# Kernel optimization log

Measured on AMD Instinct MI355X. Metric: run time of the kernel, lower is better.

Reference implementation:

```python
import jax, jax.numpy as jnp
import numpy as np

B, N, F = 8, 8192, 64          # batch of graphs, nodes per graph, feature dim
E = 1_048_576                   # total edges (avg in-degree 16 over 65536 nodes)


def setup_inputs() -> dict:
    key = jax.random.key(0)
    k1, k2, k3 = jax.random.split(key, 3)
    input_features = jax.random.normal(k1, (B, N, F), dtype=jnp.float32)
    src = jax.random.randint(k2, (E,), 0, B * N, dtype=jnp.int64)
    dst = jax.random.randint(k3, (E,), 0, B * N, dtype=jnp.int64)
    return {"input_features": input_features, "src": src, "dst": dst}


def reference(input_features, src, dst):
    # copy_src message + mean mailbox reduction (DGL update_all semantics):
    # each node's new h = mean of h over its in-neighbors; zero-in-degree
    # nodes keep their old h.
    b, n, f = input_features.shape
    num_nodes = b * n
    h = input_features.reshape(num_nodes, f)          # flatten batched graph nodes
    msg = h[src]                                       # [E, F] gathered messages
    msum = jax.ops.segment_sum(msg, dst, num_segments=num_nodes)       # [num_nodes, F]
    deg = jax.ops.segment_sum(jnp.ones((src.shape[0],), h.dtype), dst,
                              num_segments=num_nodes)                  # [num_nodes]
    mean = msum / jnp.maximum(deg, 1.0)[:, None]
    h_new = jnp.where(deg[:, None] > 0, mean, h)
    return h_new.reshape(b, n, f)
```

## Files before the change

kernel.cpp:

```cpp
#include <hip/hip_runtime.h>


#define NBUCK 2048
#define NPBLK 256
#define NPT   8
#define GBLK  1024
#define PAIRCAP 2048
#define EPBMAX 4096

template <bool BF16>
__global__ __launch_bounds__(256) void k_build(
        const float* __restrict__ h,
        const int* __restrict__ src,
        const int* __restrict__ dst,
        unsigned int* __restrict__ pairs,
        unsigned short* __restrict__ offs,
        uint4* __restrict__ hbf,
        int E, int epb, int n8) {
    int t = threadIdx.x;
    int bid = blockIdx.x;

    if (bid >= NPBLK) {
        if (!BF16) return;
        int i = (bid - NPBLK) * 256 + t;
        if (i >= n8) return;
        const float4* h4 = (const float4*)h;
        float4 a = h4[2 * i], bq = h4[2 * i + 1];
        auto pk = [](float lo, float hi) {
            unsigned int ul = __float_as_uint(lo), uh = __float_as_uint(hi);
            unsigned int rl = (ul + 0x7FFFu + ((ul >> 16) & 1u)) >> 16;
            unsigned int rh = (uh + 0x7FFFu + ((uh >> 16) & 1u)) & 0xFFFF0000u;
            return rl | rh;
        };
        hbf[i] = make_uint4(pk(a.x, a.y), pk(a.z, a.w), pk(bq.x, bq.y), pk(bq.z, bq.w));
        return;
    }

    __shared__ unsigned int hist[NBUCK];
    __shared__ uint4 dstbuf4[EPBMAX / 4];
    __shared__ unsigned int wpart[4];
    for (int i = t; i < NBUCK; i += 256) hist[i] = 0u;
    __syncthreads();

    int base = bid * epb;
    int cnt = E - base; if (cnt > epb) cnt = epb; if (cnt < 0) cnt = 0;
    int nv = cnt >> 2;

    const int4* d4 = (const int4*)(dst + base);
    for (int i = t; i < nv; i += 256) {
        int4 d = d4[i];
        dstbuf4[i] = make_uint4((unsigned)d.x, (unsigned)d.y,
                                (unsigned)d.z, (unsigned)d.w);
        atomicAdd(&hist[((unsigned)d.x) >> 5], 1u);
        atomicAdd(&hist[((unsigned)d.y) >> 5], 1u);
        atomicAdd(&hist[((unsigned)d.z) >> 5], 1u);
        atomicAdd(&hist[((unsigned)d.w) >> 5], 1u);
    }
    for (int i = nv * 4 + t; i < cnt; i += 256)
        atomicAdd(&hist[((unsigned)dst[base + i]) >> 5], 1u);
    __syncthreads();

    unsigned int loc[NPT], lsum = 0u;
    #pragma unroll
    for (int i = 0; i < NPT; ++i) { loc[i] = hist[t * NPT + i]; lsum += loc[i]; }
    int lane = t & 63, wid = t >> 6;
    unsigned int x = lsum;
    #pragma unroll
    for (int off = 1; off < 64; off <<= 1) {
        unsigned int y = __shfl_up(x, off);
        if (lane >= off) x += y;
    }
    if (lane == 63) wpart[wid] = x;
    __syncthreads();
    if (wid == 0) {
        unsigned int w = (lane < 4) ? wpart[lane] : 0u;
        #pragma unroll
        for (int off = 1; off < 4; off <<= 1) {
            unsigned int y = __shfl_up(w, off);
            if (lane >= off) w += y;
        }
        if (lane < 4) wpart[lane] = w;
    }
    __syncthreads();
    unsigned int run = (wid ? wpart[wid - 1] : 0u) + x - lsum;

    size_t orow = (size_t)bid * (NBUCK + 1);
    #pragma unroll
    for (int i = 0; i < NPT; ++i) {
        offs[orow + t * NPT + i] = (unsigned short)run;
        hist[t * NPT + i] = (unsigned)base + run;
        run += loc[i];
    }
    if (t == 255) offs[orow + NBUCK] = (unsigned short)cnt;
    __syncthreads();

    const int4* s4 = (const int4*)(src + base);
    for (int i = t; i < nv; i += 256) {
        int4 s = s4[i];
        uint4 d = dstbuf4[i];
        unsigned int p0 = atomicAdd(&hist[d.x >> 5], 1u);
        pairs[p0] = (unsigned)s.x | ((d.x & 63u) << 16);
        unsigned int p1 = atomicAdd(&hist[d.y >> 5], 1u);
        pairs[p1] = (unsigned)s.y | ((d.y & 63u) << 16);
        unsigned int p2 = atomicAdd(&hist[d.z >> 5], 1u);
        pairs[p2] = (unsigned)s.z | ((d.z & 63u) << 16);
        unsigned int p3 = atomicAdd(&hist[d.w >> 5], 1u);
        pairs[p3] = (unsigned)s.w | ((d.w & 63u) << 16);
    }
    for (int i = nv * 4 + t; i < cnt; i += 256) {
        unsigned int d = (unsigned)dst[base + i];
        unsigned int s = (unsigned)src[base + i];
        unsigned int pos = atomicAdd(&hist[d >> 5], 1u);
        pairs[pos] = s | ((d & 63u) << 16);
    }
}

template <bool BF16>
__global__ __launch_bounds__(512) void k_gather(
        const float* __restrict__ h,
        const uint2* __restrict__ hbf,
        const unsigned int* __restrict__ pairs,
        const unsigned short* __restrict__ offs,
        float* __restrict__ out, int epb) {
    __shared__ unsigned int pairbuf[PAIRCAP];
    __shared__ unsigned short ssrc[PAIRCAP];
    __shared__ unsigned int hist[64], offl[64], cur[64];
    __shared__ unsigned int wpart[8];
    int t = threadIdx.x;
    int B = blockIdx.x;
    int g = (B & 7) * (GBLK / 8) + (B >> 3);
    int b2 = 2 * g;
    if (t < 64) hist[t] = 0u;

    unsigned int s0 = 0u, mycnt = 0u;
    if (t < NPBLK) {
        size_t orow = (size_t)t * (NBUCK + 1);
        s0 = offs[orow + b2];
        unsigned int s2 = offs[orow + b2 + 2];
        mycnt = s2 - s0;
    }

    int lane = t & 63, wid = t >> 6;
    unsigned int x = mycnt;
    #pragma unroll
    for (int off = 1; off < 64; off <<= 1) {
        unsigned int y = __shfl_up(x, off);
        if (lane >= off) x += y;
    }
    if (lane == 63) wpart[wid] = x;
    __syncthreads();
    if (wid == 0) {
        unsigned int w = (lane < 8) ? wpart[lane] : 0u;
        #pragma unroll
        for (int off = 1; off < 8; off <<= 1) {
            unsigned int y = __shfl_up(w, off);
            if (lane >= off) w += y;
        }
        if (lane < 8) wpart[lane] = w;
    }
    __syncthreads();
    unsigned int mypos = (wid ? wpart[wid - 1] : 0u) + x - mycnt;
    unsigned int cnt = min(wpart[7], (unsigned)PAIRCAP);
    if (mypos >= cnt) mycnt = 0u;
    else if (mypos + mycnt > cnt) mycnt = cnt - mypos;

    for (unsigned int k = 0; k < mycnt; ++k) {
        unsigned int pr = pairs[(size_t)t * epb + s0 + k];
        pairbuf[mypos + k] = pr;
        atomicAdd(&hist[pr >> 16], 1u);
    }
    __syncthreads();

    if (t < 64) {
        unsigned int v = hist[t];
        unsigned int xx = v;
        #pragma unroll
        for (int off = 1; off < 64; off <<= 1) {
            unsigned int y = __shfl_up(xx, off);
            if (t >= off) xx += y;
        }
        offl[t] = xx - v; cur[t] = xx - v;
    }
    __syncthreads();

    for (unsigned int i = t; i < cnt; i += 512u) {
        unsigned int p = pairbuf[i];
        unsigned int pos = atomicAdd(&cur[p >> 16], 1u);
        ssrc[pos] = (unsigned short)(p & 0xFFFFu);
    }
    __syncthreads();

    int w = t >> 6;
    int egrp = lane >> 4, fq = lane & 15;
    const float4* h4 = (const float4*)h;
    float4* out4 = (float4*)out;

    for (int np = 0; np < 4; ++np) {
        int na = w * 8 + np * 2;
        int nb = na + 1;
        unsigned int sa = offl[na], da = hist[na];
        unsigned int sb = offl[nb], db = hist[nb];
        float4 accA = make_float4(0.f, 0.f, 0.f, 0.f);
        float4 accB = make_float4(0.f, 0.f, 0.f, 0.f);
        unsigned int dmax = max(da, db);
        for (unsigned int base = 0; base < dmax; base += 64u) {
            int ca = (int)min(64u, (da > base) ? (da - base) : 0u);
            int cb = (int)min(64u, (db > base) ? (db - base) : 0u);
            int ia = (lane < ca) ? (int)ssrc[sa + base + lane] : 0;
            int ib = (lane < cb) ? (int)ssrc[sb + base + lane] : 0;
            int cm = (ca > cb) ? ca : cb;
            int nit = (cm + 3) >> 2;
            for (int it = 0; it < nit; ++it) {
                int j = it * 4 + egrp;
                int sA = __shfl(ia, (j < ca) ? j : 0);
                int sB = __shfl(ib, (j < cb) ? j : 0);
                if (BF16) {
                    uint2 mA = hbf[(size_t)sA * 16 + fq];
                    uint2 mB = hbf[(size_t)sB * 16 + fq];
                    if (j < ca) {
                        accA.x += __uint_as_float(mA.x << 16);
                        accA.y += __uint_as_float(mA.x & 0xFFFF0000u);
                        accA.z += __uint_as_float(mA.y << 16);
                        accA.w += __uint_as_float(mA.y & 0xFFFF0000u);
                    }
                    if (j < cb) {
                        accB.x += __uint_as_float(mB.x << 16);
                        accB.y += __uint_as_float(mB.x & 0xFFFF0000u);
                        accB.z += __uint_as_float(mB.y << 16);
                        accB.w += __uint_as_float(mB.y & 0xFFFF0000u);
                    }
                } else {
                    float4 mA = h4[(size_t)sA * 16 + fq];
                    float4 mB = h4[(size_t)sB * 16 + fq];
                    if (j < ca) {
                        accA.x += mA.x; accA.y += mA.y; accA.z += mA.z; accA.w += mA.w;
                    }
                    if (j < cb) {
                        accB.x += mB.x; accB.y += mB.y; accB.z += mB.z; accB.w += mB.w;
                    }
                }
            }
        }
        #pragma unroll
        for (int k = 16; k <= 32; k <<= 1) {
            accA.x += __shfl_xor(accA.x, k);
            accA.y += __shfl_xor(accA.y, k);
            accA.z += __shfl_xor(accA.z, k);
            accA.w += __shfl_xor(accA.w, k);
            accB.x += __shfl_xor(accB.x, k);
            accB.y += __shfl_xor(accB.y, k);
            accB.z += __shfl_xor(accB.z, k);
            accB.w += __shfl_xor(accB.w, k);
        }
        if (lane < 32) {
            int n = (lane < 16) ? na : nb;
            unsigned int dg = (lane < 16) ? da : db;
            float4 acc = (lane < 16) ? accA : accB;
            size_t oi = ((size_t)g * 64 + n) * 16 + fq;
            float4 r;
            if (dg > 0u) {
                float inv = 1.0f / (float)dg;
                r = make_float4(acc.x * inv, acc.y * inv, acc.z * inv, acc.w * inv);
            } else {
                r = h4[oi];
            }
            out4[oi] = r;
        }
    }
}

extern "C" void kernel_launch(void* const* d_in, const int* in_sizes, int n_in,
                              void* d_out, int out_size, void* d_ws, size_t ws_size,
                              hipStream_t stream) {
    const float* h = (const float*)d_in[0];
    const int* src = (const int*)d_in[1];
    const int* dst = (const int*)d_in[2];
    float* out = (float*)d_out;
    int E = in_sizes[1];
    int nodes = out_size / 64;

    int epb = ((E + NPBLK - 1) / NPBLK + 255) & ~255;

    unsigned int* pairs  = (unsigned int*)d_ws;
    unsigned short* offs = (unsigned short*)(pairs + (size_t)NPBLK * epb);
    size_t offs_elems = (size_t)NPBLK * (NBUCK + 1);
    size_t offs_bytes = (offs_elems * 2 + 15) & ~(size_t)15;
    uint4* hbf = (uint4*)((char*)offs + offs_bytes);

    size_t need_base = (size_t)NPBLK * epb * 4 + offs_bytes;
    size_t need_bf   = need_base + (size_t)nodes * 64 * 2;
    bool use_bf = (ws_size >= need_bf);

    int n8 = nodes * 64 / 8;
    int cvtblocks = (n8 + 255) / 256;

    if (use_bf) {
        k_build<true><<<NPBLK + cvtblocks, 256, 0, stream>>>(
            h, src, dst, pairs, offs, hbf, E, epb, n8);
        k_gather<true><<<GBLK, 512, 0, stream>>>(
            h, (const uint2*)hbf, pairs, offs, out, epb);
    } else {
        k_build<false><<<NPBLK, 256, 0, stream>>>(
            h, src, dst, pairs, offs, hbf, E, epb, n8);
        k_gather<false><<<GBLK, 512, 0, stream>>>(
            h, (const uint2*)hbf, pairs, offs, out, epb);
    }
}
```

Before: 42.55 us.

## Gather 128 destination nodes per block with 1024 threads and 4-lane run loads

Each gather block now handles four buckets (128 destination nodes) instead of two, with 1024 threads, half as many blocks and a larger shared staging buffer. Pair encoding keeps 7 bits of the destination so nodes can be sorted within the larger group. Each producer run is loaded by four threads striding through it instead of one thread walking it serially, which aims to speed up the pair fetch. The trade-off is a larger shared footprint, lower block-level parallelism, and a higher risk of overflowing the pair cap.

Result: faster. 39.98 us (median of 2 runs) (-6.0%).

```diff
diff --git a/kernel.cpp b/kernel.cpp
--- a/kernel.cpp
+++ b/kernel.cpp
@@ -4,8 +4,8 @@
 #define NBUCK 2048
 #define NPBLK 256
 #define NPT   8
-#define GBLK  1024
-#define PAIRCAP 2048
+#define GBLK  512
+#define QUADCAP 4096
 #define EPBMAX 4096
 
 template <bool BF16>
@@ -99,49 +99,48 @@
         int4 s = s4[i];
         uint4 d = dstbuf4[i];
         unsigned int p0 = atomicAdd(&hist[d.x >> 5], 1u);
-        pairs[p0] = (unsigned)s.x | ((d.x & 63u) << 16);
+        pairs[p0] = (unsigned)s.x | ((d.x & 127u) << 16);
         unsigned int p1 = atomicAdd(&hist[d.y >> 5], 1u);
-        pairs[p1] = (unsigned)s.y | ((d.y & 63u) << 16);
+        pairs[p1] = (unsigned)s.y | ((d.y & 127u) << 16);
         unsigned int p2 = atomicAdd(&hist[d.z >> 5], 1u);
-        pairs[p2] = (unsigned)s.z | ((d.z & 63u) << 16);
+        pairs[p2] = (unsigned)s.z | ((d.z & 127u) << 16);
         unsigned int p3 = atomicAdd(&hist[d.w >> 5], 1u);
-        pairs[p3] = (unsigned)s.w | ((d.w & 63u) << 16);
+        pairs[p3] = (unsigned)s.w | ((d.w & 127u) << 16);
     }
     for (int i = nv * 4 + t; i < cnt; i += 256) {
         unsigned int d = (unsigned)dst[base + i];
         unsigned int s = (unsigned)src[base + i];
         unsigned int pos = atomicAdd(&hist[d >> 5], 1u);
-        pairs[pos] = s | ((d & 63u) << 16);
+        pairs[pos] = s | ((d & 127u) << 16);
     }
 }
 
 template <bool BF16>
-__global__ __launch_bounds__(512) void k_gather(
+__global__ __launch_bounds__(1024) void k_gather(
         const float* __restrict__ h,
         const uint2* __restrict__ hbf,
         const unsigned int* __restrict__ pairs,
         const unsigned short* __restrict__ offs,
         float* __restrict__ out, int epb) {
-    __shared__ unsigned int pairbuf[PAIRCAP];
-    __shared__ unsigned short ssrc[PAIRCAP];
-    __shared__ unsigned int hist[64], offl[64], cur[64];
-    __shared__ unsigned int wpart[8];
+    __shared__ unsigned int pairbuf[QUADCAP];
+    __shared__ unsigned short ssrc[QUADCAP];
+    __shared__ unsigned int hist[128], offl[128], cur[128];
+    __shared__ unsigned int wpart[16];
     int t = threadIdx.x;
     int B = blockIdx.x;
     int g = (B & 7) * (GBLK / 8) + (B >> 3);
-    int b2 = 2 * g;
-    if (t < 64) hist[t] = 0u;
-
-    unsigned int s0 = 0u, mycnt = 0u;
-    if (t < NPBLK) {
-        size_t orow = (size_t)t * (NBUCK + 1);
-        s0 = offs[orow + b2];
-        unsigned int s2 = offs[orow + b2 + 2];
-        mycnt = s2 - s0;
-    }
+    int b4 = 4 * g;
+    if (t < 128) hist[t] = 0u;
+
+    int p = t >> 2, q = t & 3;
+    size_t orow = (size_t)p * (NBUCK + 1);
+    unsigned int s0 = offs[orow + b4];
+    unsigned int s4v = offs[orow + b4 + 4];
+    unsigned int runlen = s4v - s0;
+    unsigned int contrib = (q == 0) ? runlen : 0u;
 
     int lane = t & 63, wid = t >> 6;
-    unsigned int x = mycnt;
+    unsigned int x = contrib;
     #pragma unroll
     for (int off = 1; off < 64; off <<= 1) {
         unsigned int y = __shfl_up(x, off);
@@ -150,43 +149,47 @@
     if (lane == 63) wpart[wid] = x;
     __syncthreads();
     if (wid == 0) {
-        unsigned int w = (lane < 8) ? wpart[lane] : 0u;
+        unsigned int w = (lane < 16) ? wpart[lane] : 0u;
         #pragma unroll
-        for (int off = 1; off < 8; off <<= 1) {
+        for (int off = 1; off < 16; off <<= 1) {
             unsigned int y = __shfl_up(w, off);
             if (lane >= off) w += y;
         }
-        if (lane < 8) wpart[lane] = w;
-    }
-    __syncthreads();
-    unsigned int mypos = (wid ? wpart[wid - 1] : 0u) + x - mycnt;
-    unsigned int cnt = min(wpart[7], (unsigned)PAIRCAP);
-    if (mypos >= cnt) mycnt = 0u;
-    else if (mypos + mycnt > cnt) mycnt = cnt - mypos;
-
-    for (unsigned int k = 0; k < mycnt; ++k) {
-        unsigned int pr = pairs[(size_t)t * epb + s0 + k];
+        if (lane < 16) wpart[lane] = w;
+    }
+    __syncthreads();
+    unsigned int e = (wid ? wpart[wid - 1] : 0u) + x - contrib;
+    unsigned int mypos = e - (q ? runlen : 0u);
+    unsigned int cnt = min(wpart[15], (unsigned)QUADCAP);
+    if (mypos >= cnt) runlen = 0u;
+    else if (mypos + runlen > cnt) runlen = cnt - mypos;
+
+    for (unsigned int k = (unsigned)q; k < runlen; k += 4u) {
+        unsigned int pr = pairs[(size_t)p * epb + s0 + k];
         pairbuf[mypos + k] = pr;
         atomicAdd(&hist[pr >> 16], 1u);
     }
     __syncthreads();
 
     if (t < 64) {
-        unsigned int v = hist[t];
+        unsigned int v0 = hist[2 * t], v1 = hist[2 * t + 1];
+        unsigned int v = v0 + v1;
         unsigned int xx = v;
         #pragma unroll
         for (int off = 1; off < 64; off <<= 1) {
             unsigned int y = __shfl_up(xx, off);
             if (t >= off) xx += y;
         }
-        offl[t] = xx - v; cur[t] = xx - v;
-    }
-    __syncthreads();
-
-    for (unsigned int i = t; i < cnt; i += 512u) {
-        unsigned int p = pairbuf[i];
-        unsigned int pos = atomicAdd(&cur[p >> 16], 1u);
-        ssrc[pos] = (unsigned short)(p & 0xFFFFu);
+        unsigned int excl = xx - v;
+        offl[2 * t] = excl;          cur[2 * t] = excl;
+        offl[2 * t + 1] = excl + v0; cur[2 * t + 1] = excl + v0;
+    }
+    __syncthreads();
+
+    for (unsigned int i = t; i < cnt; i += 1024u) {
+        unsigned int pr = pairbuf[i];
+        unsigned int pos = atomicAdd(&cur[pr >> 16], 1u);
+        ssrc[pos] = (unsigned short)(pr & 0xFFFFu);
     }
     __syncthreads();
 
@@ -256,7 +259,7 @@
             int n = (lane < 16) ? na : nb;
             unsigned int dg = (lane < 16) ? da : db;
             float4 acc = (lane < 16) ? accA : accB;
-            size_t oi = ((size_t)g * 64 + n) * 16 + fq;
+            size_t oi = ((size_t)g * 128 + n) * 16 + fq;
             float4 r;
             if (dg > 0u) {
                 float inv = 1.0f / (float)dg;
@@ -297,12 +300,12 @@
     if (use_bf) {
         k_build<true><<<NPBLK + cvtblocks, 256, 0, stream>>>(
             h, src, dst, pairs, offs, hbf, E, epb, n8);
-        k_gather<true><<<GBLK, 512, 0, stream>>>(
+        k_gather<true><<<GBLK, 1024, 0, stream>>>(
             h, (const uint2*)hbf, pairs, offs, out, epb);
     } else {
         k_build<false><<<NPBLK, 256, 0, stream>>>(
             h, src, dst, pairs, offs, hbf, E, epb, n8);
-        k_gather<false><<<GBLK, 512, 0, stream>>>(
+        k_gather<false><<<GBLK, 1024, 0, stream>>>(
             h, (const uint2*)hbf, pairs, offs, out, epb);
     }
 }
```
